# Kernel tuning notes

Measured on AMD Instinct MI355X. Metric: run time of the kernel, lower is better.

Reference implementation:

```python
import jax, jax.numpy as jnp
import numpy as np
import math

B, S, DIM = 2, 2048, 2048
H, HD, RD = 16, 128, 64
LKV, LQ = 512, 1536

def _rope(x, cos, sin):
    # x: (B,S,H,RD); interpret consecutive pairs as complex, multiply by e^{i theta}
    b, s, h, d = x.shape
    xr = x.reshape(b, s, h, d // 2, 2)
    xre, xim = xr[..., 0], xr[..., 1]
    c = cos[None, :, None, :]  # (1,S,1,d/2)
    sn = sin[None, :, None, :]
    ore = xre * c - xim * sn
    oim = xre * sn + xim * c
    return jnp.stack([ore, oim], axis=-1).reshape(b, s, h, d)

def setup_inputs() -> dict:
    key = jax.random.key(0)
    ks = jax.random.split(key, 12)
    def w(k, shape, fan_in):
        return jax.random.normal(k, shape, jnp.float32) * (1.0 / math.sqrt(fan_in))
    x = jax.random.normal(ks[0], (B, S, DIM), jnp.float32)
    # RoPE tables for decoupled rotary subspace of width RD
    inv_freq = 1.0 / (10000.0 ** (np.arange(0, RD, 2, dtype=np.float32) / RD))
    ang = np.outer(np.arange(S, dtype=np.float32), inv_freq)  # (S, RD/2)
    freq_cos = jnp.asarray(np.cos(ang), jnp.float32)
    freq_sin = jnp.asarray(np.sin(ang), jnp.float32)
    return {
        "x": x, "freq_cos": freq_cos, "freq_sin": freq_sin,
        "Wkv": w(ks[1], (DIM, LKV), DIM),          # latent_kv (no bias)
        "Wlq": w(ks[2], (DIM, LQ), DIM),           # latent_q (no bias)
        "Wq": w(ks[3], (LQ, H * HD), LQ),          # query (no bias)
        "Wk": w(ks[4], (LKV, H * HD), LKV),        # key (no bias)
        "Wv": w(ks[5], (LKV, H * HD), LKV),        # value (no bias)
        "Wqr": w(ks[6], (LQ, H * RD), LQ),         # decop_rot_q (bias=True)
        "bqr": jnp.zeros((H * RD,), jnp.float32),
        "Wkr": w(ks[7], (DIM, H * RD), DIM),       # decop_rot_k (bias=True)
        "bkr": jnp.zeros((H * RD,), jnp.float32),
        "Wo": w(ks[8], (H * HD, DIM), H * HD),     # out_proj (bias=True)
        "bo": jnp.zeros((DIM,), jnp.float32),
    }

def reference(x, freq_cos, freq_sin, Wkv, Wlq, Wq, Wk, Wv, Wqr, bqr, Wkr, bkr, Wo, bo):
    b, s, _ = x.shape
    cq = x @ Wlq                      # (B,S,LQ)
    ckv = x @ Wkv                     # (B,S,LKV)
    q = (cq @ Wq).reshape(b, s, H, HD)
    qr = _rope((cq @ Wqr + bqr).reshape(b, s, H, RD), freq_cos, freq_sin)
    k = (ckv @ Wk).reshape(b, s, H, HD)
    kr = _rope((x @ Wkr + bkr).reshape(b, s, H, RD), freq_cos, freq_sin)
    v = (ckv @ Wv).reshape(b, s, H, HD)
    qf = jnp.concatenate([q, qr], axis=-1)   # (B,S,H,HD+RD)
    kf = jnp.concatenate([k, kr], axis=-1)
    scale = 1.0 / math.sqrt(HD + RD)
    scores = jnp.einsum('bqhd,bkhd->bhqk', qf, kf) * scale
    # masked=True path: causal tril mask over full seq_len
    mask = jnp.tril(jnp.ones((s, s), bool))
    scores = jnp.where(mask[None, None], scores, -jnp.inf)
    att = jax.nn.softmax(scores.astype(jnp.float32), axis=-1).astype(qf.dtype)
    out = jnp.einsum('bhqk,bkhd->bqhd', att, v).reshape(b, s, H * HD)
    return out @ Wo + bo
```

## Files before the change

kernel.cpp:

```cpp
#include <hip/hip_runtime.h>
#include <hip/hip_bf16.h>
#include <stdint.h>

#define S_LEN 2048
#define NB 2
#define NH 16
#define HDIM 128
#define RDIM 64
#define DF 192
#define MROWS 4096

typedef __bf16 bf16_t;
typedef __attribute__((ext_vector_type(8))) __bf16 bf16x8;
typedef __attribute__((ext_vector_type(4))) __bf16 bf16x4;
typedef __attribute__((ext_vector_type(4))) float f32x4;
typedef __attribute__((ext_vector_type(4))) float float4v;

__device__ __forceinline__ void gload_lds16(const bf16_t* g, bf16_t* l) {
  __builtin_amdgcn_global_load_lds(
      (const __attribute__((address_space(1))) void*)g,
      (__attribute__((address_space(3))) void*)l, 16, 0, 0);
}

__global__ __launch_bounds__(256) void convert_bf16(const float* __restrict__ in,
                                                    bf16_t* __restrict__ out, int n4) {
  int i = blockIdx.x * 256 + threadIdx.x;
  if (i >= n4) return;
  float4v v = *reinterpret_cast<const float4v*>(&in[(size_t)i * 4]);
  bf16x4 o;
  o[0] = (bf16_t)v[0]; o[1] = (bf16_t)v[1]; o[2] = (bf16_t)v[2]; o[3] = (bf16_t)v[3];
  *reinterpret_cast<bf16x4*>(&out[(size_t)i * 4]) = o;
}

__global__ __launch_bounds__(256) void transpose_bf16(const float* __restrict__ in,
                                                      bf16_t* __restrict__ out,
                                                      int K, int N) {
  __shared__ float t[64][65];
  const int n0 = blockIdx.x * 64, k0 = blockIdx.y * 64;
  const int tx = threadIdx.x & 63, ty = threadIdx.x >> 6;
#pragma unroll
  for (int i = ty; i < 64; i += 4)
    t[i][tx] = in[(size_t)(k0 + i) * N + n0 + tx];
  __syncthreads();
#pragma unroll
  for (int i = ty; i < 64; i += 4)
    out[(size_t)(n0 + i) * K + k0 + tx] = (bf16_t)t[tx][i];
}

struct EpiParams {
  bf16_t* o0;
  bf16_t* o1;
  bf16_t* o2;
  float* outf;
  const float* bias;
  const float* cosb;
  const float* sinb;
};

template <int MODE>
__global__ __launch_bounds__(256) void gemm_bt(const bf16_t* __restrict__ A,
                                               const bf16_t* __restrict__ Bt,
                                               int M, int N, int K, EpiParams ep) {
  const int tid = threadIdx.x;
  const int lane = tid & 63, w = tid >> 6;
  const int l15 = lane & 15, lg = lane >> 4;
  const int gx = gridDim.x;
  const int nwg = gx * gridDim.y;
  int flat = blockIdx.y * gx + blockIdx.x;
  flat = (flat & 7) * (nwg >> 3) + (flat >> 3);
  const int m0 = (flat / gx) * 128, n0 = (flat % gx) * 128;
  const int mw = (w >> 1) * 64, nw = (w & 1) * 64;
  __shared__ alignas(16) bf16_t As[128 * 32];
  __shared__ alignas(16) bf16_t Bs[128 * 32];

  f32x4 acc[4][4] = {};
  const int row_ld = tid >> 2;
  const int col8 = (tid & 3) * 8;
  const bf16_t* ag = A + (size_t)(m0 + row_ld) * K + col8;
  const bf16_t* bg = Bt + (size_t)(n0 + row_ld) * K + col8;
  const unsigned wbase = (unsigned)(tid & ~63u) * 8;

  for (int k0 = 0; k0 < K; k0 += 32) {
    __syncthreads();
    gload_lds16(ag + k0, As + wbase);
    gload_lds16(ag + (size_t)64 * K + k0, As + 2048 + wbase);
    gload_lds16(bg + k0, Bs + wbase);
    gload_lds16(bg + (size_t)64 * K + k0, Bs + 2048 + wbase);
    __syncthreads();
    bf16x8 a[4], b[4];
#pragma unroll
    for (int i = 0; i < 4; ++i)
      a[i] = *reinterpret_cast<const bf16x8*>(&As[(mw + i * 16 + l15) * 32 + lg * 8]);
#pragma unroll
    for (int i = 0; i < 4; ++i)
      b[i] = *reinterpret_cast<const bf16x8*>(&Bs[(nw + i * 16 + l15) * 32 + lg * 8]);
#pragma unroll
    for (int i = 0; i < 4; ++i)
#pragma unroll
      for (int j = 0; j < 4; ++j)
        acc[i][j] = __builtin_amdgcn_mfma_f32_16x16x32_bf16(a[i], b[j], acc[i][j], 0, 0, 0);
  }

#pragma unroll
  for (int i = 0; i < 4; ++i)
#pragma unroll
    for (int j = 0; j < 4; ++j) {
      const int col = n0 + nw + j * 16 + l15;
#pragma unroll
      for (int r = 0; r < 4; ++r) {
        const int row = m0 + mw + i * 16 + lg * 4 + r;
        float v = acc[i][j][r];
        const int b = row >> 11, s = row & 2047;
        if constexpr (MODE == 1) {
          ep.outf[(size_t)row * N + col] = v + ep.bias[col];
        } else if constexpr (MODE == 5) {
          if (col < 1536) {
            ep.o0[(size_t)row * 1536 + col] = (bf16_t)v;
          } else if (col < 2048) {
            ep.o1[(size_t)row * 512 + (col - 1536)] = (bf16_t)v;
          } else {
            const int c2 = col - 2048;
            float vb = v + ep.bias[c2];
            float other = __shfl_xor(vb, 1, 64);
            const int h = c2 >> 6, dr = c2 & 63;
            const int fi = dr >> 1;
            const float c = ep.cosb[s * 32 + fi];
            const float sn = ep.sinb[s * 32 + fi];
            const float o = (c2 & 1) ? (other * sn + vb * c) : (vb * c - other * sn);
            ep.o2[(((size_t)(b * NH + h)) * S_LEN + s) * DF + 128 + dr] = (bf16_t)o;
          }
        } else if constexpr (MODE == 6) {
          if (col < 2048) {
            const int h = col >> 7, d = col & 127;
            ep.o0[(((size_t)(b * NH + h)) * S_LEN + s) * DF + d] = (bf16_t)v;
          } else {
            const int c2 = col - 2048;
            float vb = v + ep.bias[c2];
            float other = __shfl_xor(vb, 1, 64);
            const int h = c2 >> 6, dr = c2 & 63;
            const int fi = dr >> 1;
            const float c = ep.cosb[s * 32 + fi];
            const float sn = ep.sinb[s * 32 + fi];
            const float o = (c2 & 1) ? (other * sn + vb * c) : (vb * c - other * sn);
            ep.o0[(((size_t)(b * NH + h)) * S_LEN + s) * DF + 128 + dr] = (bf16_t)o;
          }
        } else {
          if (col < 2048) {
            const int h = col >> 7, d = col & 127;
            ep.o0[(((size_t)(b * NH + h)) * S_LEN + s) * DF + d] = (bf16_t)v;
          } else {
            const int c2 = col - 2048;
            const int h = c2 >> 7, d = c2 & 127;
            ep.o1[(((size_t)(b * NH + h)) * HDIM + d) * S_LEN + s] = (bf16_t)v;
          }
        }
      }
    }
}

__global__ __launch_bounds__(512, 4) void attn_fwd(const bf16_t* __restrict__ qf,
                                                   const bf16_t* __restrict__ kf,
                                                   const bf16_t* __restrict__ vT,
                                                   bf16_t* __restrict__ att) {
  const int tid = threadIdx.x;
  const int lane = tid & 63, w = tid >> 6;
  const int l15 = lane & 15, lg = lane >> 4;
  const int l = blockIdx.x;
  const int bh = (l & 7) * 4 + ((l >> 3) & 3);
  const int qchunk = l >> 5;
  const int qb0 = (15 - qchunk) * 128;
  const int q0 = qb0 + w * 16;
  const float scale = 0.07216878364870322f;

  __shared__ alignas(16) bf16_t Ks[64 * 192];
  __shared__ alignas(16) bf16_t Vs[128 * 64];
  __shared__ alignas(16) bf16_t Ps[8 * 16 * 64];

  const bf16_t* qptr = qf + ((size_t)bh * S_LEN + q0 + l15) * DF + lg * 8;
  bf16x8 qfr[6];
#pragma unroll
  for (int d = 0; d < 6; ++d) qfr[d] = *reinterpret_cast<const bf16x8*>(qptr + d * 32);

  f32x4 o[8] = {};
  float mrun = -1e30f, lsum = 0.0f;

  const bf16_t* kb0 = kf + (size_t)bh * S_LEN * DF;
  const bf16_t* vb0 = vT + (size_t)bh * HDIM * S_LEN;
  const int njt = qb0 / 64 + 2;
  const int wslot = tid & ~63;

  for (int jt = 0; jt < njt; ++jt) {
    const int j0 = jt * 64;
    __syncthreads();
    const bf16_t* kTile = kb0 + (size_t)j0 * DF;
#pragma unroll
    for (int i = 0; i < 3; ++i) {
      const int s = i * 512 + tid;
      const int row = s / 24;
      const int c = s - row * 24;
      const int cs = c ^ (row & 7);
      gload_lds16(kTile + (size_t)row * DF + cs * 8,
                  Ks + (size_t)(i * 512 + wslot) * 8);
    }
    const bf16_t* vTile = vb0 + j0;
#pragma unroll
    for (int i = 0; i < 2; ++i) {
      const int s = i * 512 + tid;
      const int row = s >> 3;
      const int c = s & 7;
      const int cs = c ^ (row & 7);
      gload_lds16(vTile + (size_t)row * S_LEN + cs * 8,
                  Vs + (size_t)(i * 512 + wslot) * 8);
    }
    __syncthreads();

    if (j0 > q0 + 15) continue;

    f32x4 sa[4] = {};
    __builtin_amdgcn_s_setprio(1);
#pragma unroll
    for (int jf = 0; jf < 4; ++jf) {
      const int krow = jf * 16 + l15;
      const int ksw = krow & 7;
#pragma unroll
      for (int d = 0; d < 6; ++d) {
        const int kc = (4 * d + lg) ^ ksw;
        bf16x8 kfr = *reinterpret_cast<const bf16x8*>(&Ks[krow * 192 + kc * 8]);
        sa[jf] = __builtin_amdgcn_mfma_f32_16x16x32_bf16(kfr, qfr[d], sa[jf], 0, 0, 0);
      }
    }
    __builtin_amdgcn_s_setprio(0);

    const bool full = (j0 + 63 <= q0);
    const int qi = q0 + l15;
    float sv[16];
#pragma unroll
    for (int jf = 0; jf < 4; ++jf)
#pragma unroll
      for (int r = 0; r < 4; ++r) {
        float x = sa[jf][r] * scale;
        if (!full) {
          const int j = j0 + jf * 16 + lg * 4 + r;
          if (j > qi) x = -1e30f;
        }
        sv[jf * 4 + r] = x;
      }

    float a8[8];
#pragma unroll
    for (int i = 0; i < 8; ++i) a8[i] = fmaxf(sv[i], sv[i + 8]);
#pragma unroll
    for (int i = 0; i < 4; ++i) a8[i] = fmaxf(a8[i], a8[i + 4]);
    float mx = fmaxf(fmaxf(a8[0], a8[1]), fmaxf(a8[2], a8[3]));
    mx = fmaxf(mx, __shfl_xor(mx, 16, 64));
    mx = fmaxf(mx, __shfl_xor(mx, 32, 64));

    if (__any(mx > mrun + 8.0f)) {
      const float mn = fmaxf(mrun, mx);
      const float alpha = __expf(mrun - mn);
      mrun = mn;
      lsum *= alpha;
      float af[4];
#pragma unroll
      for (int r = 0; r < 4; ++r) af[r] = __shfl(alpha, lg * 4 + r, 16);
#pragma unroll
      for (int dt = 0; dt < 8; ++dt)
#pragma unroll
        for (int r = 0; r < 4; ++r) o[dt][r] *= af[r];
    }

#pragma unroll
    for (int i = 0; i < 16; ++i) sv[i] = __expf(sv[i] - mrun);
    float s8[8];
#pragma unroll
    for (int i = 0; i < 8; ++i) s8[i] = sv[i] + sv[i + 8];
#pragma unroll
    for (int i = 0; i < 4; ++i) s8[i] = s8[i] + s8[i + 4];
    float sm = (s8[0] + s8[1]) + (s8[2] + s8[3]);
    sm += __shfl_xor(sm, 16, 64);
    sm += __shfl_xor(sm, 32, 64);
    lsum += sm;

#pragma unroll
    for (int jf = 0; jf < 4; ++jf) {
      bf16x4 pk;
#pragma unroll
      for (int r = 0; r < 4; ++r) pk[r] = (bf16_t)sv[jf * 4 + r];
      const int key = jf * 16 + lg * 4;
      *reinterpret_cast<bf16x4*>(
          &Ps[w * 1024 + l15 * 64 + (key ^ ((l15 & 7) << 3))]) = pk;
    }
    asm volatile("s_waitcnt lgkmcnt(0)" ::: "memory");
    __builtin_amdgcn_sched_barrier(0);
    bf16x8 pfr[2];
#pragma unroll
    for (int jk = 0; jk < 2; ++jk)
      pfr[jk] = *reinterpret_cast<const bf16x8*>(
          &Ps[w * 1024 + l15 * 64 + (((jk * 4 + lg) ^ (l15 & 7)) << 3)]);

    __builtin_amdgcn_s_setprio(1);
#pragma unroll
    for (int dt = 0; dt < 8; ++dt) {
      const int vrow = dt * 16 + l15;
      const int vsw = vrow & 7;
#pragma unroll
      for (int jk = 0; jk < 2; ++jk) {
        const int vc = (jk * 4 + lg) ^ vsw;
        bf16x8 vfr = *reinterpret_cast<const bf16x8*>(&Vs[vrow * 64 + vc * 8]);
        o[dt] = __builtin_amdgcn_mfma_f32_16x16x32_bf16(pfr[jk], vfr, o[dt], 0, 0, 0);
      }
    }
    __builtin_amdgcn_s_setprio(0);
  }

  const float inv = 1.0f / lsum;
  float iv[4];
#pragma unroll
  for (int r = 0; r < 4; ++r) iv[r] = __shfl(inv, lg * 4 + r, 16);
  const int b = bh >> 4, h = bh & 15;
#pragma unroll
  for (int dt = 0; dt < 8; ++dt)
#pragma unroll
    for (int r = 0; r < 4; ++r) {
      const int s = q0 + lg * 4 + r;
      att[((size_t)b * S_LEN + s) * 2048 + h * 128 + dt * 16 + l15] =
          (bf16_t)(o[dt][r] * iv[r]);
    }
}

extern "C" void kernel_launch(void* const* d_in, const int* in_sizes, int n_in,
                              void* d_out, int out_size, void* d_ws, size_t ws_size,
                              hipStream_t stream) {
  const float* x    = (const float*)d_in[0];
  const float* fcos = (const float*)d_in[1];
  const float* fsin = (const float*)d_in[2];
  const float* Wkv  = (const float*)d_in[3];
  const float* Wlq  = (const float*)d_in[4];
  const float* Wq   = (const float*)d_in[5];
  const float* Wk   = (const float*)d_in[6];
  const float* Wv   = (const float*)d_in[7];
  const float* Wqr  = (const float*)d_in[8];
  const float* bqr  = (const float*)d_in[9];
  const float* Wkr  = (const float*)d_in[10];
  const float* bkr  = (const float*)d_in[11];
  const float* Wo   = (const float*)d_in[12];
  const float* bo   = (const float*)d_in[13];
  float* out = (float*)d_out;

  char* ws = (char*)d_ws;
  size_t off = 0;
  auto alloc = [&](size_t bytes) {
    void* p = ws + off;
    off += (bytes + 255) & ~(size_t)255;
    return p;
  };
  bf16_t* xb    = (bf16_t*)alloc((size_t)MROWS * 2048 * 2);
  bf16_t* WcatA = (bf16_t*)alloc((size_t)3072 * 2048 * 2);
  bf16_t* WcatB = (bf16_t*)alloc((size_t)3072 * 1536 * 2);
  bf16_t* WcatC = (bf16_t*)alloc((size_t)4096 * 512 * 2);
  bf16_t* WoT   = (bf16_t*)alloc((size_t)2048 * 2048 * 2);
  bf16_t* cq    = (bf16_t*)alloc((size_t)MROWS * 1536 * 2);
  bf16_t* ckv   = (bf16_t*)alloc((size_t)MROWS * 512 * 2);
  bf16_t* qfb   = (bf16_t*)alloc((size_t)NB * NH * S_LEN * DF * 2);
  bf16_t* kfb   = (bf16_t*)alloc((size_t)NB * NH * S_LEN * DF * 2);
  bf16_t* vTb   = (bf16_t*)alloc((size_t)NB * NH * HDIM * S_LEN * 2);
  bf16_t* attb  = (bf16_t*)alloc((size_t)MROWS * 2048 * 2);

  {
    int n4 = (MROWS * 2048) / 4;
    convert_bf16<<<dim3((n4 + 255) / 256), dim3(256), 0, stream>>>(x, xb, n4);
  }
  auto tr = [&](const float* in, bf16_t* o_, int K, int N) {
    transpose_bf16<<<dim3(N / 64, K / 64), dim3(256), 0, stream>>>(in, o_, K, N);
  };
  tr(Wlq, WcatA, 2048, 1536);
  tr(Wkv, WcatA + (size_t)1536 * 2048, 2048, 512);
  tr(Wkr, WcatA + (size_t)2048 * 2048, 2048, 1024);
  tr(Wq,  WcatB, 1536, 2048);
  tr(Wqr, WcatB + (size_t)2048 * 1536, 1536, 1024);
  tr(Wk,  WcatC, 512, 2048);
  tr(Wv,  WcatC + (size_t)2048 * 512, 512, 2048);
  tr(Wo,  WoT, 2048, 2048);

  EpiParams ep{};

  ep = {cq, ckv, kfb, nullptr, bkr, fcos, fsin};
  gemm_bt<5><<<dim3(3072 / 128, MROWS / 128), dim3(256), 0, stream>>>(
      xb, WcatA, MROWS, 3072, 2048, ep);
  ep = {qfb, nullptr, nullptr, nullptr, bqr, fcos, fsin};
  gemm_bt<6><<<dim3(3072 / 128, MROWS / 128), dim3(256), 0, stream>>>(
      cq, WcatB, MROWS, 3072, 1536, ep);
  ep = {kfb, vTb, nullptr, nullptr, nullptr, nullptr, nullptr};
  gemm_bt<7><<<dim3(4096 / 128, MROWS / 128), dim3(256), 0, stream>>>(
      ckv, WcatC, MROWS, 4096, 512, ep);
  attn_fwd<<<dim3(512), dim3(512), 0, stream>>>(qfb, kfb, vTb, attb);
  ep = {nullptr, nullptr, nullptr, out, bo, nullptr, nullptr};
  gemm_bt<1><<<dim3(2048 / 128, MROWS / 128), dim3(256), 0, stream>>>(
      attb, WoT, MROWS, 2048, 2048, ep);
}
```

Measured before the change: 389.2 us.

## Batch weight transposes, merge two GEMMs, and give each attention wave two query tiles

Result: faster. 364.9 us (-6.2%).

```diff
diff --git a/kernel.cpp b/kernel.cpp
--- a/kernel.cpp
+++ b/kernel.cpp
@@ -32,19 +32,26 @@
   *reinterpret_cast<bf16x4*>(&out[(size_t)i * 4]) = o;
 }
 
-__global__ __launch_bounds__(256) void transpose_bf16(const float* __restrict__ in,
-                                                      bf16_t* __restrict__ out,
-                                                      int K, int N) {
+struct TrDesc { const float* src; bf16_t* dst; int K; int N; int nbx; int base; };
+struct TrPack { TrDesc d[8]; };
+
+__global__ __launch_bounds__(256) void transpose_all(TrPack p) {
   __shared__ float t[64][65];
-  const int n0 = blockIdx.x * 64, k0 = blockIdx.y * 64;
+  const int bid = blockIdx.x;
+  int m = 0;
+#pragma unroll
+  for (int i = 1; i < 8; ++i) m += (bid >= p.d[i].base);
+  const TrDesc td = p.d[m];
+  const int local = bid - td.base;
+  const int n0 = (local % td.nbx) * 64, k0 = (local / td.nbx) * 64;
   const int tx = threadIdx.x & 63, ty = threadIdx.x >> 6;
 #pragma unroll
   for (int i = ty; i < 64; i += 4)
-    t[i][tx] = in[(size_t)(k0 + i) * N + n0 + tx];
+    t[i][tx] = td.src[(size_t)(k0 + i) * td.N + n0 + tx];
   __syncthreads();
 #pragma unroll
   for (int i = ty; i < 64; i += 4)
-    out[(size_t)(n0 + i) * K + k0 + tx] = (bf16_t)t[tx][i];
+    td.dst[(size_t)(n0 + i) * td.K + k0 + tx] = (bf16_t)t[tx][i];
 }
 
 struct EpiParams {
@@ -58,20 +65,14 @@
 };
 
 template <int MODE>
-__global__ __launch_bounds__(256) void gemm_bt(const bf16_t* __restrict__ A,
-                                               const bf16_t* __restrict__ Bt,
-                                               int M, int N, int K, EpiParams ep) {
+__device__ __forceinline__ void gemm_body(const bf16_t* __restrict__ A,
+                                          const bf16_t* __restrict__ Bt,
+                                          int N, int K, int m0, int n0,
+                                          bf16_t* As, bf16_t* Bs, EpiParams ep) {
   const int tid = threadIdx.x;
   const int lane = tid & 63, w = tid >> 6;
   const int l15 = lane & 15, lg = lane >> 4;
-  const int gx = gridDim.x;
-  const int nwg = gx * gridDim.y;
-  int flat = blockIdx.y * gx + blockIdx.x;
-  flat = (flat & 7) * (nwg >> 3) + (flat >> 3);
-  const int m0 = (flat / gx) * 128, n0 = (flat % gx) * 128;
   const int mw = (w >> 1) * 64, nw = (w & 1) * 64;
-  __shared__ alignas(16) bf16_t As[128 * 32];
-  __shared__ alignas(16) bf16_t Bs[128 * 32];
 
   f32x4 acc[4][4] = {};
   const int row_ld = tid >> 2;
@@ -158,7 +159,41 @@
     }
 }
 
-__global__ __launch_bounds__(512, 4) void attn_fwd(const bf16_t* __restrict__ qf,
+template <int MODE>
+__global__ __launch_bounds__(256) void gemm_bt(const bf16_t* __restrict__ A,
+                                               const bf16_t* __restrict__ Bt,
+                                               int N, int K, EpiParams ep) {
+  __shared__ alignas(16) bf16_t As[128 * 32];
+  __shared__ alignas(16) bf16_t Bs[128 * 32];
+  const int gx = gridDim.x;
+  const int nwg = gx * gridDim.y;
+  int flat = blockIdx.y * gx + blockIdx.x;
+  flat = (flat & 7) * (nwg >> 3) + (flat >> 3);
+  const int m0 = (flat / gx) * 128, n0 = (flat % gx) * 128;
+  gemm_body<MODE>(A, Bt, N, K, m0, n0, As, Bs, ep);
+}
+
+__global__ __launch_bounds__(256) void gemm_bt67(const bf16_t* __restrict__ A6,
+                                                 const bf16_t* __restrict__ Bt6,
+                                                 const bf16_t* __restrict__ A7,
+                                                 const bf16_t* __restrict__ Bt7,
+                                                 EpiParams ep6, EpiParams ep7) {
+  __shared__ alignas(16) bf16_t As[128 * 32];
+  __shared__ alignas(16) bf16_t Bs[128 * 32];
+  const int bid = blockIdx.x;
+  if (bid < 768) {
+    int flat = (bid & 7) * 96 + (bid >> 3);
+    const int m0 = (flat / 24) * 128, n0 = (flat % 24) * 128;
+    gemm_body<6>(A6, Bt6, 3072, 1536, m0, n0, As, Bs, ep6);
+  } else {
+    int b2 = bid - 768;
+    int flat = (b2 & 7) * 128 + (b2 >> 3);
+    const int m0 = (flat / 32) * 128, n0 = (flat % 32) * 128;
+    gemm_body<7>(A7, Bt7, 4096, 512, m0, n0, As, Bs, ep7);
+  }
+}
+
+__global__ __launch_bounds__(256, 2) void attn_fwd(const bf16_t* __restrict__ qf,
                                                    const bf16_t* __restrict__ kf,
                                                    const bf16_t* __restrict__ vT,
                                                    bf16_t* __restrict__ att) {
@@ -169,20 +204,24 @@
   const int bh = (l & 7) * 4 + ((l >> 3) & 3);
   const int qchunk = l >> 5;
   const int qb0 = (15 - qchunk) * 128;
-  const int q0 = qb0 + w * 16;
+  const int q0 = qb0 + w * 32;
   const float scale = 0.07216878364870322f;
 
   __shared__ alignas(16) bf16_t Ks[64 * 192];
   __shared__ alignas(16) bf16_t Vs[128 * 64];
-  __shared__ alignas(16) bf16_t Ps[8 * 16 * 64];
-
-  const bf16_t* qptr = qf + ((size_t)bh * S_LEN + q0 + l15) * DF + lg * 8;
-  bf16x8 qfr[6];
-#pragma unroll
-  for (int d = 0; d < 6; ++d) qfr[d] = *reinterpret_cast<const bf16x8*>(qptr + d * 32);
-
-  f32x4 o[8] = {};
-  float mrun = -1e30f, lsum = 0.0f;
+  __shared__ alignas(16) bf16_t Ps[4 * 2048];
+
+  bf16x8 qfr[2][6];
+#pragma unroll
+  for (int mf = 0; mf < 2; ++mf) {
+    const bf16_t* qptr = qf + ((size_t)bh * S_LEN + q0 + mf * 16 + l15) * DF + lg * 8;
+#pragma unroll
+    for (int d = 0; d < 6; ++d)
+      qfr[mf][d] = *reinterpret_cast<const bf16x8*>(qptr + d * 32);
+  }
+
+  f32x4 o[2][8] = {};
+  float mrun[2] = {-1e30f, -1e30f}, lsum[2] = {0.0f, 0.0f};
 
   const bf16_t* kb0 = kf + (size_t)bh * S_LEN * DF;
   const bf16_t* vb0 = vT + (size_t)bh * HDIM * S_LEN;
@@ -194,29 +233,29 @@
     __syncthreads();
     const bf16_t* kTile = kb0 + (size_t)j0 * DF;
 #pragma unroll
-    for (int i = 0; i < 3; ++i) {
-      const int s = i * 512 + tid;
+    for (int i = 0; i < 6; ++i) {
+      const int s = i * 256 + tid;
       const int row = s / 24;
       const int c = s - row * 24;
       const int cs = c ^ (row & 7);
       gload_lds16(kTile + (size_t)row * DF + cs * 8,
-                  Ks + (size_t)(i * 512 + wslot) * 8);
+                  Ks + (size_t)(i * 256 + wslot) * 8);
     }
     const bf16_t* vTile = vb0 + j0;
 #pragma unroll
-    for (int i = 0; i < 2; ++i) {
-      const int s = i * 512 + tid;
+    for (int i = 0; i < 4; ++i) {
+      const int s = i * 256 + tid;
       const int row = s >> 3;
       const int c = s & 7;
       const int cs = c ^ (row & 7);
       gload_lds16(vTile + (size_t)row * S_LEN + cs * 8,
-                  Vs + (size_t)(i * 512 + wslot) * 8);
+                  Vs + (size_t)(i * 256 + wslot) * 8);
     }
     __syncthreads();
 
-    if (j0 > q0 + 15) continue;
-
-    f32x4 sa[4] = {};
+    if (j0 > q0 + 31) continue;
+
+    f32x4 sa[2][4] = {};
     __builtin_amdgcn_s_setprio(1);
 #pragma unroll
     for (int jf = 0; jf < 4; ++jf) {
@@ -226,77 +265,85 @@
       for (int d = 0; d < 6; ++d) {
         const int kc = (4 * d + lg) ^ ksw;
         bf16x8 kfr = *reinterpret_cast<const bf16x8*>(&Ks[krow * 192 + kc * 8]);
-        sa[jf] = __builtin_amdgcn_mfma_f32_16x16x32_bf16(kfr, qfr[d], sa[jf], 0, 0, 0);
+#pragma unroll
+        for (int mf = 0; mf < 2; ++mf)
+          sa[mf][jf] =
+              __builtin_amdgcn_mfma_f32_16x16x32_bf16(kfr, qfr[mf][d], sa[mf][jf], 0, 0, 0);
       }
     }
     __builtin_amdgcn_s_setprio(0);
 
-    const bool full = (j0 + 63 <= q0);
-    const int qi = q0 + l15;
-    float sv[16];
-#pragma unroll
-    for (int jf = 0; jf < 4; ++jf)
-#pragma unroll
-      for (int r = 0; r < 4; ++r) {
-        float x = sa[jf][r] * scale;
-        if (!full) {
-          const int j = j0 + jf * 16 + lg * 4 + r;
-          if (j > qi) x = -1e30f;
+#pragma unroll
+    for (int mf = 0; mf < 2; ++mf) {
+      const int qi = q0 + mf * 16 + l15;
+      const bool full = (j0 + 63 <= q0 + mf * 16);
+      float sv[16];
+#pragma unroll
+      for (int jf = 0; jf < 4; ++jf)
+#pragma unroll
+        for (int r = 0; r < 4; ++r) {
+          float x = sa[mf][jf][r] * scale;
+          if (!full) {
+            const int j = j0 + jf * 16 + lg * 4 + r;
+            if (j > qi) x = -1e30f;
+          }
+          sv[jf * 4 + r] = x;
         }
-        sv[jf * 4 + r] = x;
-      }
-
-    float a8[8];
-#pragma unroll
-    for (int i = 0; i < 8; ++i) a8[i] = fmaxf(sv[i], sv[i + 8]);
-#pragma unroll
-    for (int i = 0; i < 4; ++i) a8[i] = fmaxf(a8[i], a8[i + 4]);
-    float mx = fmaxf(fmaxf(a8[0], a8[1]), fmaxf(a8[2], a8[3]));
-    mx = fmaxf(mx, __shfl_xor(mx, 16, 64));
-    mx = fmaxf(mx, __shfl_xor(mx, 32, 64));
-
-    if (__any(mx > mrun + 8.0f)) {
-      const float mn = fmaxf(mrun, mx);
-      const float alpha = __expf(mrun - mn);
-      mrun = mn;
-      lsum *= alpha;
-      float af[4];
-#pragma unroll
-      for (int r = 0; r < 4; ++r) af[r] = __shfl(alpha, lg * 4 + r, 16);
-#pragma unroll
-      for (int dt = 0; dt < 8; ++dt)
-#pragma unroll
-        for (int r = 0; r < 4; ++r) o[dt][r] *= af[r];
-    }
-
-#pragma unroll
-    for (int i = 0; i < 16; ++i) sv[i] = __expf(sv[i] - mrun);
-    float s8[8];
-#pragma unroll
-    for (int i = 0; i < 8; ++i) s8[i] = sv[i] + sv[i + 8];
-#pragma unroll
-    for (int i = 0; i < 4; ++i) s8[i] = s8[i] + s8[i + 4];
-    float sm = (s8[0] + s8[1]) + (s8[2] + s8[3]);
-    sm += __shfl_xor(sm, 16, 64);
-    sm += __shfl_xor(sm, 32, 64);
-    lsum += sm;
-
-#pragma unroll
-    for (int jf = 0; jf < 4; ++jf) {
-      bf16x4 pk;
-#pragma unroll
-      for (int r = 0; r < 4; ++r) pk[r] = (bf16_t)sv[jf * 4 + r];
-      const int key = jf * 16 + lg * 4;
-      *reinterpret_cast<bf16x4*>(
-          &Ps[w * 1024 + l15 * 64 + (key ^ ((l15 & 7) << 3))]) = pk;
+
+      float a8[8];
+#pragma unroll
+      for (int i = 0; i < 8; ++i) a8[i] = fmaxf(sv[i], sv[i + 8]);
+#pragma unroll
+      for (int i = 0; i < 4; ++i) a8[i] = fmaxf(a8[i], a8[i + 4]);
+      float mx = fmaxf(fmaxf(a8[0], a8[1]), fmaxf(a8[2], a8[3]));
+      mx = fmaxf(mx, __shfl_xor(mx, 16, 64));
+      mx = fmaxf(mx, __shfl_xor(mx, 32, 64));
+
+      if (__any(mx > mrun[mf] + 8.0f)) {
+        const float mn = fmaxf(mrun[mf], mx);
+        const float alpha = __expf(mrun[mf] - mn);
+        mrun[mf] = mn;
+        lsum[mf] *= alpha;
+        float af[4];
+#pragma unroll
+        for (int r = 0; r < 4; ++r) af[r] = __shfl(alpha, lg * 4 + r, 16);
+#pragma unroll
+        for (int dt = 0; dt < 8; ++dt)
+#pragma unroll
+          for (int r = 0; r < 4; ++r) o[mf][dt][r] *= af[r];
+      }
+
+#pragma unroll
+      for (int i = 0; i < 16; ++i) sv[i] = __expf(sv[i] - mrun[mf]);
+      float s8[8];
+#pragma unroll
+      for (int i = 0; i < 8; ++i) s8[i] = sv[i] + sv[i + 8];
+#pragma unroll
+      for (int i = 0; i < 4; ++i) s8[i] = s8[i] + s8[i + 4];
+      float sm = (s8[0] + s8[1]) + (s8[2] + s8[3]);
+      sm += __shfl_xor(sm, 16, 64);
+      sm += __shfl_xor(sm, 32, 64);
+      lsum[mf] += sm;
+
+#pragma unroll
+      for (int jf = 0; jf < 4; ++jf) {
+        bf16x4 pk;
+#pragma unroll
+        for (int r = 0; r < 4; ++r) pk[r] = (bf16_t)sv[jf * 4 + r];
+        const int key = jf * 16 + lg * 4;
+        *reinterpret_cast<bf16x4*>(
+            &Ps[w * 2048 + mf * 1024 + l15 * 64 + (key ^ ((l15 & 7) << 3))]) = pk;
+      }
     }
     asm volatile("s_waitcnt lgkmcnt(0)" ::: "memory");
     __builtin_amdgcn_sched_barrier(0);
-    bf16x8 pfr[2];
-#pragma unroll
-    for (int jk = 0; jk < 2; ++jk)
-      pfr[jk] = *reinterpret_cast<const bf16x8*>(
-          &Ps[w * 1024 + l15 * 64 + (((jk * 4 + lg) ^ (l15 & 7)) << 3)]);
+    bf16x8 pfr[2][2];
+#pragma unroll
+    for (int mf = 0; mf < 2; ++mf)
+#pragma unroll
+      for (int jk = 0; jk < 2; ++jk)
+        pfr[mf][jk] = *reinterpret_cast<const bf16x8*>(
+            &Ps[w * 2048 + mf * 1024 + l15 * 64 + (((jk * 4 + lg) ^ (l15 & 7)) << 3)]);
 
     __builtin_amdgcn_s_setprio(1);
 #pragma unroll
@@ -307,25 +354,31 @@
       for (int jk = 0; jk < 2; ++jk) {
         const int vc = (jk * 4 + lg) ^ vsw;
         bf16x8 vfr = *reinterpret_cast<const bf16x8*>(&Vs[vrow * 64 + vc * 8]);
-        o[dt] = __builtin_amdgcn_mfma_f32_16x16x32_bf16(pfr[jk], vfr, o[dt], 0, 0, 0);
+#pragma unroll
+        for (int mf = 0; mf < 2; ++mf)
+          o[mf][dt] =
+              __builtin_amdgcn_mfma_f32_16x16x32_bf16(pfr[mf][jk], vfr, o[mf][dt], 0, 0, 0);
       }
     }
     __builtin_amdgcn_s_setprio(0);
   }
 
-  const float inv = 1.0f / lsum;
-  float iv[4];
-#pragma unroll
-  for (int r = 0; r < 4; ++r) iv[r] = __shfl(inv, lg * 4 + r, 16);
   const int b = bh >> 4, h = bh & 15;
 #pragma unroll
-  for (int dt = 0; dt < 8; ++dt)
-#pragma unroll
-    for (int r = 0; r < 4; ++r) {
-      const int s = q0 + lg * 4 + r;
-      att[((size_t)b * S_LEN + s) * 2048 + h * 128 + dt * 16 + l15] =
-          (bf16_t)(o[dt][r] * iv[r]);
-    }
+  for (int mf = 0; mf < 2; ++mf) {
+    const float inv = 1.0f / lsum[mf];
+    float iv[4];
+#pragma unroll
+    for (int r = 0; r < 4; ++r) iv[r] = __shfl(inv, lg * 4 + r, 16);
+#pragma unroll
+    for (int dt = 0; dt < 8; ++dt)
+#pragma unroll
+      for (int r = 0; r < 4; ++r) {
+        const int s = q0 + mf * 16 + lg * 4 + r;
+        att[((size_t)b * S_LEN + s) * 2048 + h * 128 + dt * 16 + l15] =
+            (bf16_t)(o[mf][dt][r] * iv[r]);
+      }
+  }
 }
 
 extern "C" void kernel_launch(void* const* d_in, const int* in_sizes, int n_in,
@@ -370,31 +423,34 @@
     int n4 = (MROWS * 2048) / 4;
     convert_bf16<<<dim3((n4 + 255) / 256), dim3(256), 0, stream>>>(x, xb, n4);
   }
-  auto tr = [&](const float* in, bf16_t* o_, int K, int N) {
-    transpose_bf16<<<dim3(N / 64, K / 64), dim3(256), 0, stream>>>(in, o_, K, N);
-  };
-  tr(Wlq, WcatA, 2048, 1536);
-  tr(Wkv, WcatA + (size_t)1536 * 2048, 2048, 512);
-  tr(Wkr, WcatA + (size_t)2048 * 2048, 2048, 1024);
-  tr(Wq,  WcatB, 1536, 2048);
-  tr(Wqr, WcatB + (size_t)2048 * 1536, 1536, 1024);
-  tr(Wk,  WcatC, 512, 2048);
-  tr(Wv,  WcatC + (size_t)2048 * 512, 512, 2048);
-  tr(Wo,  WoT, 2048, 2048);
-
-  EpiParams ep{};
+  {
+    TrPack p;
+    int base = 0;
+    auto set = [&](int i, const float* s, bf16_t* d, int K, int N) {
+      p.d[i] = {s, d, K, N, N / 64, base};
+      base += (N / 64) * (K / 64);
+    };
+    set(0, Wlq, WcatA, 2048, 1536);
+    set(1, Wkv, WcatA + (size_t)1536 * 2048, 2048, 512);
+    set(2, Wkr, WcatA + (size_t)2048 * 2048, 2048, 1024);
+    set(3, Wq,  WcatB, 1536, 2048);
+    set(4, Wqr, WcatB + (size_t)2048 * 1536, 1536, 1024);
+    set(5, Wk,  WcatC, 512, 2048);
+    set(6, Wv,  WcatC + (size_t)2048 * 512, 512, 2048);
+    set(7, Wo,  WoT, 2048, 2048);
+    transpose_all<<<dim3(base), dim3(256), 0, stream>>>(p);
+  }
+
+  EpiParams ep{}, ep2{};
 
   ep = {cq, ckv, kfb, nullptr, bkr, fcos, fsin};
   gemm_bt<5><<<dim3(3072 / 128, MROWS / 128), dim3(256), 0, stream>>>(
-      xb, WcatA, MROWS, 3072, 2048, ep);
-  ep = {qfb, nullptr, nullptr, nullptr, bqr, fcos, fsin};
-  gemm_bt<6><<<dim3(3072 / 128, MROWS / 128), dim3(256), 0, stream>>>(
-      cq, WcatB, MROWS, 3072, 1536, ep);
-  ep = {kfb, vTb, nullptr, nullptr, nullptr, nullptr, nullptr};
-  gemm_bt<7><<<dim3(4096 / 128, MROWS / 128), dim3(256), 0, stream>>>(
-      ckv, WcatC, MROWS, 4096, 512, ep);
-  attn_fwd<<<dim3(512), dim3(512), 0, stream>>>(qfb, kfb, vTb, attb);
+      xb, WcatA, 3072, 2048, ep);
+  ep  = {qfb, nullptr, nullptr, nullptr, bqr, fcos, fsin};
+  ep2 = {kfb, vTb, nullptr, nullptr, nullptr, nullptr, nullptr};
+  gemm_bt67<<<dim3(1792), dim3(256), 0, stream>>>(cq, WcatB, ckv, WcatC, ep, ep2);
+  attn_fwd<<<dim3(512), dim3(256), 0, stream>>>(qfb, kfb, vTb, attb);
   ep = {nullptr, nullptr, nullptr, out, bo, nullptr, nullptr};
   gemm_bt<1><<<dim3(2048 / 128, MROWS / 128), dim3(256), 0, stream>>>(
-      attb, WoT, MROWS, 2048, 2048, ep);
-}
+      attb, WoT, 2048, 2048, ep);
+}
```
